# Kernel optimization log

Hardware: AMD Instinct MI355X
Metric: run time of the kernel (lower is better)

## Reference

```python
import jax, jax.numpy as jnp
import numpy as np

B, S, D = 8, 1024, 1024
NEG = -1e9


def setup_inputs() -> dict:
    key = jax.random.key(0)
    ks = jax.random.split(key, 6)
    context = jax.random.normal(ks[0], (B, S, D), dtype=jnp.float32)
    eos_mask = jax.random.randint(ks[1], (B, S, S), 0, 2).astype(jnp.int32)
    scale = 1.0 / np.sqrt(D).astype(np.float32)
    Wq = jax.random.normal(ks[2], (D, D), dtype=jnp.float32) * scale
    bq = jnp.zeros((D,), jnp.float32)
    Wk = jax.random.normal(ks[3], (D, D), dtype=jnp.float32) * scale
    bk = jnp.zeros((D,), jnp.float32)
    ln_a = jnp.ones((D,), jnp.float32)
    ln_b = jnp.zeros((D,), jnp.float32)
    return dict(context=context, eos_mask=eos_mask, Wq=Wq, bq=bq, Wk=Wk, bk=bk,
                ln_a=ln_a, ln_b=ln_b)


def _forward(context, eos_mask, Wq, bq, Wk, bk, ln_a, ln_b):
    d_model = context.shape[-1]
    seq_len = context.shape[1]
    # LayerNorm with torch-style unbiased std (ddof=1)
    mean = context.mean(-1, keepdims=True)
    var = ((context - mean) ** 2).sum(-1, keepdims=True) / (d_model - 1)
    x = ln_a * (context - mean) / (jnp.sqrt(var) + 1e-6) + ln_b

    a = jnp.eye(seq_len, k=1, dtype=jnp.int32)    # super-diagonal
    b = jnp.eye(seq_len, k=0, dtype=jnp.int32)    # diagonal
    c = jnp.eye(seq_len, k=-1, dtype=jnp.int32)   # sub-diagonal
    tri = jnp.triu(jnp.ones((seq_len, seq_len), jnp.float32), 0)

    mask = eos_mask & (a + c)  # [B,S,S] banded + eos mask

    q = x @ Wq.T + bq
    k = x @ Wk.T + bk
    scores = jnp.einsum('bsd,btd->bst', q, k) / d_model
    scores = jnp.where(mask == 0, NEG, scores)
    neibor = jax.nn.softmax(scores, axis=-1)
    neibor = jnp.sqrt(neibor * jnp.swapaxes(neibor, -2, -1) + 1e-9)

    # log-space triangular matmul 'scan'
    t = jnp.where(a == 0, 0.0, jnp.log(neibor + 1e-9)) @ tri  # [B,S,S]
    g = jnp.exp(jnp.einsum('st,btu->bsu', tri, t))
    strict_upper = tri.astype(jnp.int32) - b
    g = jnp.where(strict_upper == 0, 0.0, g)
    g = g + jnp.swapaxes(g, -2, -1) + jnp.where(b == 0, 1e-9, neibor)
    return g, neibor


def reference(context, eos_mask, Wq, bq, Wk, bk, ln_a, ln_b):
    return _forward(context, eos_mask, Wq, bq, Wk, bk, ln_a, ln_b)
```

## Files before the change

### kernel.cpp

```cpp
#include <hip/hip_runtime.h>
#include <math.h>

#define B_ 8
#define S_ 1024
#define D_ 1024
constexpr int BS = B_ * S_;

typedef short bf16x8 __attribute__((ext_vector_type(8)));
typedef float f32x4 __attribute__((ext_vector_type(4)));

__device__ __forceinline__ unsigned short f2bf(float f) {
    unsigned int u = __float_as_uint(f);
    u += 0x7fffu + ((u >> 16) & 1u);
    return (unsigned short)(u >> 16);
}
__device__ __forceinline__ float bf2f(unsigned short h) {
    return __uint_as_float(((unsigned int)h) << 16);
}

__device__ __forceinline__ float block_reduce_sum(float val, float* sh) {
    int tid = threadIdx.x;
    int lane = tid & 63, w = tid >> 6;
    #pragma unroll
    for (int off = 32; off > 0; off >>= 1) val += __shfl_down(val, off, 64);
    if (lane == 0) sh[w] = val;
    __syncthreads();
    int nw = blockDim.x >> 6;
    float total = 0.f;
    for (int i = 0; i < nw; i++) total += sh[i];
    __syncthreads();
    return total;
}

__global__ void ln_kernel(const float* __restrict__ ctx,
                          const float* __restrict__ ln_a,
                          const float* __restrict__ ln_b,
                          const float* __restrict__ u,
                          const float* __restrict__ v,
                          unsigned short* __restrict__ xb,
                          float* __restrict__ au, float* __restrict__ av) {
    __shared__ float sh[4];
    int r = blockIdx.x;
    int tid = threadIdx.x;
    int d0 = tid * 4;
    const float* row = ctx + (size_t)r * D_;
    float4 x4 = *(const float4*)(row + d0);
    float s = x4.x + x4.y + x4.z + x4.w;
    float total = block_reduce_sum(s, sh);
    float mean = total * (1.0f / D_);
    float dx = x4.x - mean, dy = x4.y - mean, dz = x4.z - mean, dw = x4.w - mean;
    float sq = dx * dx + dy * dy + dz * dz + dw * dw;
    float varsum = block_reduce_sum(sq, sh);
    float var = varsum * (1.0f / (D_ - 1));
    float inv = 1.0f / (sqrtf(var) + 1e-6f);
    float4 a4 = *(const float4*)(ln_a + d0);
    float4 b4 = *(const float4*)(ln_b + d0);
    float y0 = a4.x * dx * inv + b4.x;
    float y1 = a4.y * dy * inv + b4.y;
    float y2 = a4.z * dz * inv + b4.z;
    float y3 = a4.w * dw * inv + b4.w;
    ushort4 o;
    o.x = f2bf(y0); o.y = f2bf(y1); o.z = f2bf(y2); o.w = f2bf(y3);
    *(ushort4*)(xb + (size_t)r * D_ + d0) = o;
    float4 u4 = *(const float4*)(u + d0);
    float4 v4 = *(const float4*)(v + d0);
    float pu = u4.x * y0 + u4.y * y1 + u4.z * y2 + u4.w * y3;
    float pv = v4.x * y0 + v4.y * y1 + v4.z * y2 + v4.w * y3;
    pu = block_reduce_sum(pu, sh);
    pv = block_reduce_sum(pv, sh);
    if (tid == 0) { au[r] = pu; av[r] = pv; }
}

__global__ void prep_kernel(const float* __restrict__ Wq, const float* __restrict__ Wk,
                            const float* __restrict__ bq, const float* __restrict__ bk,
                            unsigned short* __restrict__ Wqt,
                            unsigned short* __restrict__ Wkt,
                            float* __restrict__ u, float* __restrict__ v,
                            float* __restrict__ c0) {
    int bid = blockIdx.x;
    int tid = threadIdx.x;
    if (bid < 2048) {
        __shared__ float t[32][33];
        const float* in = (bid < 1024) ? Wq : Wk;
        unsigned short* out = (bid < 1024) ? Wqt : Wkt;
        int bb = bid & 1023;
        int bx = (bb & 31) * 32, by = (bb >> 5) * 32;
        int tx = tid & 31, ty = tid >> 5;
        #pragma unroll
        for (int i = 0; i < 32; i += 8)
            t[ty + i][tx] = in[(size_t)(by + ty + i) * D_ + bx + tx];
        __syncthreads();
        #pragma unroll
        for (int i = 0; i < 32; i += 8)
            out[(size_t)(bx + ty + i) * D_ + by + tx] = f2bf(t[tx][ty + i]);
    } else {
        int b = bid - 2048;
        float ua[4] = {}, va[4] = {};
        int d0 = b * 128;
        for (int d = d0; d < d0 + 128; d++) {
            float bqd = bq[d], bkd = bk[d];
            const float* wkr = Wk + (size_t)d * D_;
            const float* wqr = Wq + (size_t)d * D_;
            #pragma unroll
            for (int i = 0; i < 4; i++) {
                int c = tid + i * 256;
                ua[i] += wkr[c] * bqd;
                va[i] += wqr[c] * bkd;
            }
        }
        #pragma unroll
        for (int i = 0; i < 4; i++) {
            atomicAdd(&u[tid + i * 256], ua[i]);
            atomicAdd(&v[tid + i * 256], va[i]);
        }
        if (tid < 128) atomicAdd(c0, bq[d0 + tid] * bk[d0 + tid]);
    }
}

__global__ __launch_bounds__(256) void gemm_bt64(
    const unsigned short* __restrict__ A,
    const unsigned short* __restrict__ Bt,
    unsigned short* __restrict__ C,
    int M, int N, int K) {
    __shared__ __align__(16) unsigned short As[64 * 64];
    __shared__ __align__(16) unsigned short Bs[64 * 64];
    const int tid = threadIdx.x;
    const int wave = tid >> 6, lane = tid & 63;
    const int bm = blockIdx.y * 64, bn = blockIdx.x * 64;
    const int lrow8 = lane >> 3;
    const int pchunk = lane & 7;
    const int m_lane = lane & 15, quad = lane >> 4;
    const int wr = wave >> 1, wc = wave & 1;

    f32x4 acc[2][2] = {};

    for (int k0 = 0; k0 < K; k0 += 64) {
        #pragma unroll
        for (int c = 0; c < 2; c++) {
            int row = wave * 16 + c * 8 + lrow8;
            int gchunk = pchunk ^ (row & 7);
            const unsigned short* gpA = A + (size_t)(bm + row) * K + k0 + gchunk * 8;
            const unsigned short* gpB = Bt + (size_t)(bn + row) * K + k0 + gchunk * 8;
            __builtin_amdgcn_global_load_lds(
                (const __attribute__((address_space(1))) void*)gpA,
                (__attribute__((address_space(3))) void*)(As + (wave * 16 + c * 8) * 64),
                16, 0, 0);
            __builtin_amdgcn_global_load_lds(
                (const __attribute__((address_space(1))) void*)gpB,
                (__attribute__((address_space(3))) void*)(Bs + (wave * 16 + c * 8) * 64),
                16, 0, 0);
        }
        __syncthreads();
        #pragma unroll
        for (int kk = 0; kk < 2; kk++) {
            bf16x8 af[2], bfr[2];
            #pragma unroll
            for (int i = 0; i < 2; i++) {
                int row = wr * 32 + i * 16 + m_lane;
                int lchunk = kk * 4 + quad;
                af[i] = *(const bf16x8*)(As + row * 64 + (lchunk ^ (row & 7)) * 8);
            }
            #pragma unroll
            for (int j = 0; j < 2; j++) {
                int row = wc * 32 + j * 16 + m_lane;
                int lchunk = kk * 4 + quad;
                bfr[j] = *(const bf16x8*)(Bs + row * 64 + (lchunk ^ (row & 7)) * 8);
            }
            #pragma unroll
            for (int i = 0; i < 2; i++)
                #pragma unroll
                for (int j = 0; j < 2; j++)
                    acc[i][j] = __builtin_amdgcn_mfma_f32_16x16x32_bf16(
                        af[i], bfr[j], acc[i][j], 0, 0, 0);
        }
        __syncthreads();
    }
    #pragma unroll
    for (int i = 0; i < 2; i++)
        #pragma unroll
        for (int j = 0; j < 2; j++)
            #pragma unroll
            for (int r = 0; r < 4; r++) {
                int row = bm + wr * 32 + i * 16 + quad * 4 + r;
                int col = bn + wc * 32 + j * 16 + m_lane;
                C[(size_t)row * N + col] = f2bf(acc[i][j][r]);
            }
}

__global__ __launch_bounds__(256) void gemm_fused(
    const unsigned short* __restrict__ A,
    const unsigned short* __restrict__ Bt,
    float* __restrict__ ydu, float* __restrict__ ydd,
    int M, int N, int K) {
    __shared__ __align__(16) unsigned short smem[17408];
    unsigned short* As = smem;
    unsigned short* Bs = smem + 128 * 64;
    const int tid = threadIdx.x;
    const int wave = tid >> 6, lane = tid & 63;
    const int bid = blockIdx.x;
    const int sk = bid >> 9;
    const int b2 = bid & 511;
    const int bm = (b2 & 63) * 128, bn = (b2 >> 6) * 128;
    const int lrow8 = lane >> 3;
    const int pchunk = lane & 7;
    const int m_lane = lane & 15, quad = lane >> 4;
    const int wr = wave >> 1, wc = wave & 1;

    f32x4 acc[4][4] = {};

    const int khalf = K >> 1;
    const int kbeg = sk * khalf, kend = kbeg + khalf;
    for (int k0 = kbeg; k0 < kend; k0 += 64) {
        #pragma unroll
        for (int c = 0; c < 4; c++) {
            int row = wave * 32 + c * 8 + lrow8;
            int gchunk = pchunk ^ (row & 7);
            const unsigned short* gpA = A + (size_t)(bm + row) * K + k0 + gchunk * 8;
            __builtin_amdgcn_global_load_lds(
                (const __attribute__((address_space(1))) void*)gpA,
                (__attribute__((address_space(3))) void*)(As + (wave * 32 + c * 8) * 64),
                16, 0, 0);
            const unsigned short* gpB = Bt + (size_t)(bn + row) * K + k0 + gchunk * 8;
            __builtin_amdgcn_global_load_lds(
                (const __attribute__((address_space(1))) void*)gpB,
                (__attribute__((address_space(3))) void*)(Bs + (wave * 32 + c * 8) * 64),
                16, 0, 0);
        }
        __syncthreads();
        #pragma unroll
        for (int kk = 0; kk < 2; kk++) {
            bf16x8 af[4], bfr[4];
            #pragma unroll
            for (int i = 0; i < 4; i++) {
                int row = wr * 64 + i * 16 + m_lane;
                int lchunk = kk * 4 + quad;
                af[i] = *(const bf16x8*)(As + row * 64 + (lchunk ^ (row & 7)) * 8);
            }
            #pragma unroll
            for (int j = 0; j < 4; j++) {
                int row = wc * 64 + j * 16 + m_lane;
                int lchunk = kk * 4 + quad;
                bfr[j] = *(const bf16x8*)(Bs + row * 64 + (lchunk ^ (row & 7)) * 8);
            }
            #pragma unroll
            for (int i = 0; i < 4; i++)
                #pragma unroll
                for (int j = 0; j < 4; j++)
                    acc[i][j] = __builtin_amdgcn_mfma_f32_16x16x32_bf16(
                        af[i], bfr[j], acc[i][j], 0, 0, 0);
        }
        __syncthreads();
    }

    unsigned short* Xs = smem;
    #pragma unroll
    for (int it = 0; it < 8; it++) {
        int idx = it * 256 + tid;
        int lr = idx >> 4;
        int ch = idx & 15;
        *(bf16x8*)(Xs + lr * 136 + ch * 8) =
            *(const bf16x8*)(A + (size_t)(bm + lr) * K + bn + ch * 8);
    }
    __syncthreads();

    #pragma unroll
    for (int i = 0; i < 4; i++) {
        #pragma unroll
        for (int r = 0; r < 4; r++) {
            int lrow = wr * 64 + i * 16 + quad * 4 + r;
            int row = bm + lrow;
            int s = row & (S_ - 1);
            bool hu = (s < S_ - 1), hd = (s > 0);
            float pu = 0.f, pd = 0.f;
            #pragma unroll
            for (int j = 0; j < 4; j++) {
                int lc = wc * 64 + j * 16 + m_lane;
                float a = acc[i][j][r];
                if (hu) {
                    float xu = (lrow < 127) ? bf2f(Xs[(lrow + 1) * 136 + lc])
                                            : bf2f(A[(size_t)(row + 1) * K + bn + lc]);
                    pu += a * xu;
                }
                if (hd) {
                    float xd = (lrow > 0) ? bf2f(Xs[(lrow - 1) * 136 + lc])
                                          : bf2f(A[(size_t)(row - 1) * K + bn + lc]);
                    pd += a * xd;
                }
            }
            #pragma unroll
            for (int off = 1; off < 16; off <<= 1) {
                pu += __shfl_xor(pu, off, 64);
                pd += __shfl_xor(pd, off, 64);
            }
            if (m_lane == 0) {
                atomicAdd(&ydu[row], pu);
                atomicAdd(&ydd[row], pd);
            }
        }
    }
}

__global__ void softmax_prefix(const float* __restrict__ ydu, const float* __restrict__ ydd,
                               const float* __restrict__ au, const float* __restrict__ av,
                               const float* __restrict__ c0p, const int* __restrict__ eos,
                               float* __restrict__ Pup, float* __restrict__ Pdn,
                               float* __restrict__ bg, double* __restrict__ C) {
    __shared__ float pdsh[1024];
    __shared__ double wsum[16];
    int b = blockIdx.x;
    int t = threadIdx.x;
    int r = b * S_ + t;
    float c0 = *c0p;
    const float inv_d = 1.0f / D_;
    bool mu = false, md = false;
    float su = 0.f, sd = 0.f;
    if (t < S_ - 1) {
        mu = eos[(size_t)b * S_ * S_ + (size_t)t * S_ + (t + 1)] != 0;
        su = (ydu[r] + av[r] + au[r + 1] + c0) * inv_d;
    }
    if (t > 0) {
        md = eos[(size_t)b * S_ * S_ + (size_t)t * S_ + (t - 1)] != 0;
        sd = (ydd[r] + av[r] + au[r - 1] + c0) * inv_d;
    }
    float pu, pd, pb;
    if (mu && md) {
        float m = fmaxf(su, sd);
        float eu = expf(su - m), ed = expf(sd - m);
        float inv = 1.0f / (eu + ed);
        pu = eu * inv; pd = ed * inv; pb = 0.f;
    } else if (mu) { pu = 1.f; pd = 0.f; pb = 0.f; }
    else if (md)   { pu = 0.f; pd = 1.f; pb = 0.f; }
    else           { pu = pd = pb = 1.0f / S_; }
    Pup[r] = pu; Pdn[r] = pd; bg[r] = pb;
    pdsh[t] = pd;
    __syncthreads();
    double l = 0.0;
    if (t < S_ - 1) {
        float p = sqrtf(pu * pdsh[t + 1] + 1e-9f) + 1e-9f;
        l = log((double)p);
    }
    int lane = t & 63, w = t >> 6;
    double vv = l;
    #pragma unroll
    for (int off = 1; off < 64; off <<= 1) {
        double o = __shfl_up(vv, off, 64);
        if (lane >= off) vv += o;
    }
    if (lane == 63) wsum[w] = vv;
    __syncthreads();
    if (t == 0) {
        double acc = 0.0;
        #pragma unroll
        for (int i = 0; i < 16; i++) { double x = wsum[i]; wsum[i] = acc; acc += x; }
    }
    __syncthreads();
    vv += wsum[w];
    size_t base = (size_t)b * S_;
    if (t == 0) C[base] = 0.0;
    if (t < S_ - 1) C[base + t + 1] = vv;
}

__global__ void write_out(const float* __restrict__ Pup, const float* __restrict__ Pdn,
                          const float* __restrict__ bg, const double* __restrict__ C,
                          float* __restrict__ out) {
    int r = blockIdx.x;
    int b = r >> 10, s = r & (S_ - 1);
    size_t rowbase = (size_t)r * S_;
    size_t bb = (size_t)b * S_;
    float pu_s = (s < S_ - 1) ? Pup[r] : 0.f;
    float pd_s = (s > 0) ? Pdn[r] : 0.f;
    float bg_s = bg[r];
    double C_s = C[r];
    int t0 = threadIdx.x * 4;
    float* gp = out;
    float* np = out + (size_t)B_ * S_ * S_;
    float4 bgv = *(const float4*)(bg + bb + t0);
    float4 gv, nv;
    #pragma unroll
    for (int j = 0; j < 4; j++) {
        int t = t0 + j;
        float P_st = (t == s + 1) ? pu_s : ((t == s - 1) ? pd_s : bg_s);
        float P_ts;
        if (t == s - 1)      P_ts = Pup[bb + t];
        else if (t == s + 1) P_ts = Pdn[bb + t];
        else                 P_ts = ((const float*)&bgv)[j];
        float neib = sqrtf(P_st * P_ts + 1e-9f);
        float g;
        if (t == s) {
            g = neib;
        } else {
            double diff = (t > s) ? (C[bb + t] - C_s) : (C_s - C[bb + t]);
            g = expf((float)diff) + 1e-9f;
        }
        ((float*)&gv)[j] = g;
        ((float*)&nv)[j] = neib;
    }
    *(float4*)(gp + rowbase + t0) = gv;
    *(float4*)(np + rowbase + t0) = nv;
}

extern "C" void kernel_launch(void* const* d_in, const int* in_sizes, int n_in,
                              void* d_out, int out_size, void* d_ws, size_t ws_size,
                              hipStream_t stream) {
    const float* ctx  = (const float*)d_in[0];
    const int*   eos  = (const int*)d_in[1];
    const float* Wq   = (const float*)d_in[2];
    const float* bq   = (const float*)d_in[3];
    const float* Wk   = (const float*)d_in[4];
    const float* bk   = (const float*)d_in[5];
    const float* ln_a = (const float*)d_in[6];
    const float* ln_b = (const float*)d_in[7];
    float* out = (float*)d_out;

    char* ws = (char*)d_ws;
    size_t off = 0;
    auto alloc = [&](size_t bytes) {
        void* p = ws + off;
        off += (bytes + 255) & ~(size_t)255;
        return p;
    };
    unsigned short* Xb  = (unsigned short*)alloc((size_t)BS * D_ * 2);
    unsigned short* Wqt = (unsigned short*)alloc((size_t)D_ * D_ * 2);
    unsigned short* Wkt = (unsigned short*)alloc((size_t)D_ * D_ * 2);
    unsigned short* Mt  = (unsigned short*)alloc((size_t)D_ * D_ * 2);
    float*  ydu = (float*)alloc(BS * 4);
    float*  ydd = (float*)alloc(BS * 4);
    float*  u   = (float*)alloc(D_ * 4);
    float*  v   = (float*)alloc(D_ * 4);
    float*  c0  = (float*)alloc(4);
    size_t zero_bytes = (size_t)((char*)c0 - (char*)ydu) + 256;
    float*  au  = (float*)alloc(BS * 4);
    float*  av  = (float*)alloc(BS * 4);
    float*  Pup = (float*)alloc(BS * 4);
    float*  Pdn = (float*)alloc(BS * 4);
    float*  bg  = (float*)alloc(BS * 4);
    double* Cp  = (double*)alloc(BS * 8);

    hipMemsetAsync(ydu, 0, zero_bytes, stream);
    prep_kernel<<<2056, 256, 0, stream>>>(Wq, Wk, bq, bk, Wqt, Wkt, u, v, c0);
    ln_kernel<<<BS, 256, 0, stream>>>(ctx, ln_a, ln_b, u, v, Xb, au, av);
    gemm_bt64<<<dim3(16, 16), 256, 0, stream>>>(Wkt, Wqt, Mt, D_, D_, D_);
    gemm_fused<<<1024, 256, 0, stream>>>(Xb, Mt, ydu, ydd, BS, D_, D_);
    softmax_prefix<<<B_, 1024, 0, stream>>>(ydu, ydd, au, av, c0, eos, Pup, Pdn, bg, Cp);
    write_out<<<BS, 256, 0, stream>>>(Pup, Pdn, bg, Cp, out);
}
```

Before: 234.6 us.

## Spread bias projection across more blocks and async-load epilogue tile into swizzled LDS

The bias-vector part of prep_kernel goes from 8 blocks of 128 rows each to 128 blocks of 8 rows, plus one dedicated block that reduces bq·bk. This shortens the serial tail of the prep kernel at the cost of more atomics on u and v. In gemm_fused, the epilogue neighbor-row tile is now loaded with global_load_lds direct-to-LDS transfers into an XOR-swizzled layout instead of a padded one. This removes the register round-trip and trims shared memory usage.

New measurement: 220.9 us. 1.06x faster.

```diff
diff --git a/kernel.cpp b/kernel.cpp
--- a/kernel.cpp
+++ b/kernel.cpp
@@ -95,25 +95,36 @@
             out[(size_t)(bx + ty + i) * D_ + by + tx] = f2bf(t[tx][ty + i]);
     } else {
         int b = bid - 2048;
-        float ua[4] = {}, va[4] = {};
-        int d0 = b * 128;
-        for (int d = d0; d < d0 + 128; d++) {
-            float bqd = bq[d], bkd = bk[d];
-            const float* wkr = Wk + (size_t)d * D_;
-            const float* wqr = Wq + (size_t)d * D_;
+        if (b == 128) {
+            __shared__ float sh2[4];
+            float p = 0.f;
             #pragma unroll
             for (int i = 0; i < 4; i++) {
-                int c = tid + i * 256;
-                ua[i] += wkr[c] * bqd;
-                va[i] += wqr[c] * bkd;
-            }
-        }
-        #pragma unroll
-        for (int i = 0; i < 4; i++) {
-            atomicAdd(&u[tid + i * 256], ua[i]);
-            atomicAdd(&v[tid + i * 256], va[i]);
-        }
-        if (tid < 128) atomicAdd(c0, bq[d0 + tid] * bk[d0 + tid]);
+                int d = tid + i * 256;
+                p += bq[d] * bk[d];
+            }
+            float tot = block_reduce_sum(p, sh2);
+            if (tid == 0) atomicAdd(c0, tot);
+        } else {
+            float ua[4] = {}, va[4] = {};
+            int d0 = b * 8;
+            for (int d = d0; d < d0 + 8; d++) {
+                float bqd = bq[d], bkd = bk[d];
+                const float* wkr = Wk + (size_t)d * D_;
+                const float* wqr = Wq + (size_t)d * D_;
+                #pragma unroll
+                for (int i = 0; i < 4; i++) {
+                    int c = tid + i * 256;
+                    ua[i] += wkr[c] * bqd;
+                    va[i] += wqr[c] * bkd;
+                }
+            }
+            #pragma unroll
+            for (int i = 0; i < 4; i++) {
+                atomicAdd(&u[tid + i * 256], ua[i]);
+                atomicAdd(&v[tid + i * 256], va[i]);
+            }
+        }
     }
 }
 
@@ -187,12 +198,16 @@
             }
 }
 
+__device__ __forceinline__ int xs_idx(int row, int col) {
+    return row * 128 + (((col >> 3) ^ (row & 7)) << 3) + (col & 7);
+}
+
 __global__ __launch_bounds__(256) void gemm_fused(
     const unsigned short* __restrict__ A,
     const unsigned short* __restrict__ Bt,
     float* __restrict__ ydu, float* __restrict__ ydd,
     int M, int N, int K) {
-    __shared__ __align__(16) unsigned short smem[17408];
+    __shared__ __align__(16) unsigned short smem[16384];
     unsigned short* As = smem;
     unsigned short* Bs = smem + 128 * 64;
     const int tid = threadIdx.x;
@@ -255,11 +270,15 @@
     unsigned short* Xs = smem;
     #pragma unroll
     for (int it = 0; it < 8; it++) {
-        int idx = it * 256 + tid;
-        int lr = idx >> 4;
-        int ch = idx & 15;
-        *(bf16x8*)(Xs + lr * 136 + ch * 8) =
-            *(const bf16x8*)(A + (size_t)(bm + lr) * K + bn + ch * 8);
+        int c = it * 256 + wave * 64 + lane;
+        int lr = c >> 4;
+        int ch = c & 15;
+        int gch = ch ^ (lr & 7);
+        const unsigned short* gp = A + (size_t)(bm + lr) * K + bn + gch * 8;
+        __builtin_amdgcn_global_load_lds(
+            (const __attribute__((address_space(1))) void*)gp,
+            (__attribute__((address_space(3))) void*)(Xs + (size_t)(it * 256 + wave * 64) * 8),
+            16, 0, 0);
     }
     __syncthreads();
 
@@ -277,12 +296,12 @@
                 int lc = wc * 64 + j * 16 + m_lane;
                 float a = acc[i][j][r];
                 if (hu) {
-                    float xu = (lrow < 127) ? bf2f(Xs[(lrow + 1) * 136 + lc])
+                    float xu = (lrow < 127) ? bf2f(Xs[xs_idx(lrow + 1, lc)])
                                             : bf2f(A[(size_t)(row + 1) * K + bn + lc]);
                     pu += a * xu;
                 }
                 if (hd) {
-                    float xd = (lrow > 0) ? bf2f(Xs[(lrow - 1) * 136 + lc])
+                    float xd = (lrow > 0) ? bf2f(Xs[xs_idx(lrow - 1, lc)])
                                           : bf2f(A[(size_t)(row - 1) * K + bn + lc]);
                     pd += a * xd;
                 }
@@ -437,7 +456,7 @@
     double* Cp  = (double*)alloc(BS * 8);
 
     hipMemsetAsync(ydu, 0, zero_bytes, stream);
-    prep_kernel<<<2056, 256, 0, stream>>>(Wq, Wk, bq, bk, Wqt, Wkt, u, v, c0);
+    prep_kernel<<<2177, 256, 0, stream>>>(Wq, Wk, bq, bk, Wqt, Wkt, u, v, c0);
     ln_kernel<<<BS, 256, 0, stream>>>(ctx, ln_a, ln_b, u, v, Xb, au, av);
     gemm_bt64<<<dim3(16, 16), 256, 0, stream>>>(Wkt, Wqt, Mt, D_, D_, D_);
     gemm_fused<<<1024, 256, 0, stream>>>(Xb, Mt, ydu, ydd, BS, D_, D_);
```
